# Kernel optimization log

Hardware: AMD Instinct MI355X
Metric: run time of the kernel (lower is better)

The kernel has to match this reference:

```python
import jax, jax.numpy as jnp
import numpy as np

B, T, C = 2, 2048, 1024
N_HEAD, D_HEAD = 16, 64


def setup_inputs() -> dict:
    key = jax.random.key(0)
    k1, k2, k3 = jax.random.split(key, 3)
    scale_in = 1.0 / np.sqrt(C)
    return {
        "x": jax.random.normal(k1, (B, T, C), dtype=jnp.float32),
        "W_attn": jax.random.normal(k2, (C, 3 * C), dtype=jnp.float32) * scale_in,
        "b_attn": jnp.zeros((3 * C,), dtype=jnp.float32),
        "W_proj": jax.random.normal(k3, (C, C), dtype=jnp.float32) * scale_in,
        "b_proj": jnp.zeros((C,), dtype=jnp.float32),
    }


def reference(x, W_attn, b_attn, W_proj, b_proj):
    Bx, Tx, Cx = x.shape
    qkv = x @ W_attn + b_attn                       # [B,T,3C]
    q, k, v = jnp.split(qkv, 3, axis=-1)
    # [B,T,C] -> [B,H,T,Dh]
    q = q.reshape(Bx, Tx, N_HEAD, D_HEAD).transpose(0, 2, 1, 3)
    k = k.reshape(Bx, Tx, N_HEAD, D_HEAD).transpose(0, 2, 1, 3)
    v = v.reshape(Bx, Tx, N_HEAD, D_HEAD).transpose(0, 2, 1, 3)
    att = jnp.einsum("bhqd,bhkd->bhqk", q, k) * (1.0 / jnp.sqrt(D_HEAD))
    causal_mask = jnp.tril(jnp.ones((Tx, Tx), dtype=jnp.bool_))[None, None]
    att = jnp.where(causal_mask, att, -jnp.inf)
    att = jax.nn.softmax(att, axis=-1)
    y = jnp.einsum("bhqk,bhkd->bhqd", att, v)        # [B,H,T,Dh]
    y = y.transpose(0, 2, 1, 3).reshape(Bx, Tx, Cx)  # [B,T,C]
    return y @ W_proj + b_proj
```

## Files before the change

### kernel.cpp

```cpp
#include <hip/hip_runtime.h>

#define BB 2
#define TT 2048
#define CC 1024
#define NHEAD 16
#define DHEAD 64

typedef __attribute__((ext_vector_type(8))) short short8;
typedef __attribute__((ext_vector_type(8))) unsigned short ushort8;
typedef __attribute__((ext_vector_type(4))) float floatx4;
typedef __attribute__((ext_vector_type(2))) unsigned int uintx2;

__device__ inline unsigned short f32_to_bf16_rne(float f) {
  unsigned u = __builtin_bit_cast(unsigned, f);
  unsigned r = (u + 0x7FFFu + ((u >> 16) & 1u)) >> 16;
  return (unsigned short)r;
}
__device__ inline unsigned cvt_pk_bf16(float lo, float hi) {
  unsigned r;
  asm("v_cvt_pk_bf16_f32 %0, %1, %2" : "=v"(r) : "v"(lo), "v"(hi));
  return r;
}
__device__ inline void gload_lds16(const void* g, void* l) {
  __builtin_amdgcn_global_load_lds(
      (const __attribute__((address_space(1))) void*)g,
      (__attribute__((address_space(3))) void*)l, 16, 0, 0);
}

__device__ inline void transpose_tile(const float* __restrict__ W,
                                      unsigned short* __restrict__ Wt,
                                      int K, int N, int scale_cut, float scl,
                                      int bx, int by, float (*T)[33]) {
  const int tx = threadIdx.x & 31;
  const int ty = threadIdx.x >> 5;
  const int r0 = by * 32, c0 = bx * 32;
#pragma unroll
  for (int i = 0; i < 4; ++i)
    T[ty + i * 8][tx] = W[(size_t)(r0 + ty + i * 8) * N + c0 + tx];
  __syncthreads();
#pragma unroll
  for (int i = 0; i < 4; ++i) {
    const int nrow = c0 + ty + i * 8;
    const float s = (nrow < scale_cut) ? scl : 1.0f;
    Wt[(size_t)nrow * K + r0 + tx] = f32_to_bf16_rne(T[tx][ty + i * 8] * s);
  }
}

__global__ __launch_bounds__(256) void prep_kernel(
    const float* __restrict__ x, const float* __restrict__ W_attn,
    const float* __restrict__ b_attn, const float* __restrict__ W_proj,
    unsigned short* __restrict__ xb, unsigned short* __restrict__ Wat,
    unsigned short* __restrict__ Wpt, float* __restrict__ bscl, float scl) {
  __shared__ float T[32][33];
  const int id = blockIdx.x;
  if (id < 4096) {
    const int i = (id * 256 + threadIdx.x) * 4;
    float4 v = *(const float4*)(x + i);
    ushort4 o;
    o.x = f32_to_bf16_rne(v.x);
    o.y = f32_to_bf16_rne(v.y);
    o.z = f32_to_bf16_rne(v.z);
    o.w = f32_to_bf16_rne(v.w);
    *(ushort4*)(xb + i) = o;
  } else if (id < 4096 + 3072) {
    const int t = id - 4096;
    transpose_tile(W_attn, Wat, CC, 3 * CC, CC, scl, t % 96, t / 96, T);
  } else if (id < 4096 + 3072 + 1024) {
    const int t = id - (4096 + 3072);
    transpose_tile(W_proj, Wpt, CC, CC, 0, 1.0f, t % 32, t / 32, T);
  } else {
    const int i = (id - 8192) * 256 + threadIdx.x;
    if (i < 3 * CC) bscl[i] = b_attn[i] * (i < CC ? scl : 1.0f);
  }
}

__global__ __launch_bounds__(256) void transpose_v_kernel(
    const unsigned short* __restrict__ qkv, unsigned short* __restrict__ vT) {
  __shared__ unsigned short Ts[64][72];
  const int tt0 = blockIdx.x * 64;
  const int bh = blockIdx.y;
  const int h = bh & (NHEAD - 1);
  const int b = bh >> 4;
  const int tid = threadIdx.x;
  const unsigned short* src = qkv + (size_t)(b * TT) * (3 * CC) + 2 * CC + h * DHEAD;
#pragma unroll
  for (int it = 0; it < 2; ++it) {
    const int t = it * 32 + (tid >> 3);
    const int d8 = (tid & 7) * 8;
    ushort8 v = *(const ushort8*)(src + (size_t)(tt0 + t) * (3 * CC) + d8);
#pragma unroll
    for (int j = 0; j < 8; ++j) Ts[t][d8 + j] = v[j];
  }
  __syncthreads();
  unsigned short* dst = vT + ((size_t)((b * NHEAD + h) * DHEAD)) * TT;
#pragma unroll
  for (int it = 0; it < 2; ++it) {
    const int d = it * 32 + (tid >> 3);
    const int t8 = (tid & 7) * 8;
    ushort8 o;
#pragma unroll
    for (int j = 0; j < 8; ++j) o[j] = Ts[t8 + j][d];
    *(ushort8*)(dst + (size_t)d * TT + tt0 + t8) = o;
  }
}

__global__ __launch_bounds__(512, 2) void gemm256_kernel(
    const unsigned short* __restrict__ A,
    const unsigned short* __restrict__ Bt,
    const float* __restrict__ bias,
    unsigned short* __restrict__ C,
    int M, int N, int K) {
  __shared__ unsigned short SA[3][256 * 32];
  __shared__ unsigned short SB[3][256 * 32];

  const int id = blockIdx.x;
  const int xcd = id & 7;
  const int j = id >> 3;
  const int row0 = (xcd * 2 + (j >= 12 ? 1 : 0)) * 256;
  const int col0 = (j % 12) * 256;

  const int tid = threadIdx.x;
  const int w = tid >> 6;
  const int lane = tid & 63;
  const int l15 = lane & 15;
  const int l4 = lane >> 4;
  const int wr = (w >> 2) * 128;
  const int wc = (w & 3) * 64;
  const int sr = lane >> 2;
  const int sc = lane & 3;

  floatx4 acc[8][4];
#pragma unroll
  for (int m = 0; m < 8; ++m)
#pragma unroll
    for (int n = 0; n < 4; ++n) acc[m][n] = (floatx4){0.f, 0.f, 0.f, 0.f};

  auto stageA = [&](int t) {
    const int buf = t % 3;
    const int k0 = t * 32;
#pragma unroll
    for (int l = 0; l < 2; ++l) {
      const int r = w * 16 + sr + l * 128;
      gload_lds16(A + (size_t)(row0 + r) * K + k0 + ((sc ^ ((r >> 1) & 3)) * 8),
                  (char*)SA[buf] + (w * 16 + l * 128) * 64);
    }
  };
  auto stageB = [&](int t) {
    const int buf = t % 3;
    const int k0 = t * 32;
#pragma unroll
    for (int l = 0; l < 2; ++l) {
      const int r = w * 16 + sr + l * 128;
      gload_lds16(Bt + (size_t)(col0 + r) * K + k0 + ((sc ^ ((r >> 1) & 3)) * 8),
                  (char*)SB[buf] + (w * 16 + l * 128) * 64);
    }
  };

  stageA(0); stageB(0);
  stageA(1); stageB(1);
  asm volatile("s_waitcnt vmcnt(4)" ::: "memory");
  __builtin_amdgcn_s_barrier();

  const int NT = K / 32;
  for (int t = 0; t < NT; ++t) {
    const unsigned short* sa = SA[t % 3];
    const unsigned short* sb = SB[t % 3];

    short8 af[4], bf[4];
#pragma unroll
    for (int n = 0; n < 4; ++n) {
      const int rb = wc + n * 16 + l15;
      bf[n] = *(const short8*)(sb + rb * 32 + ((l4 ^ ((rb >> 1) & 3)) * 8));
    }
#pragma unroll
    for (int m = 0; m < 4; ++m) {
      const int ra = wr + m * 16 + l15;
      af[m] = *(const short8*)(sa + ra * 32 + ((l4 ^ ((ra >> 1) & 3)) * 8));
    }
    if (t + 2 < NT) stageA(t + 2);
    __builtin_amdgcn_s_barrier();
    __builtin_amdgcn_s_setprio(1);
#pragma unroll
    for (int m = 0; m < 4; ++m)
#pragma unroll
      for (int n = 0; n < 4; ++n)
        acc[m][n] = __builtin_amdgcn_mfma_f32_16x16x32_bf16(af[m], bf[n], acc[m][n], 0, 0, 0);
    __builtin_amdgcn_s_setprio(0);
    __builtin_amdgcn_s_barrier();

#pragma unroll
    for (int m = 0; m < 4; ++m) {
      const int ra = wr + 64 + m * 16 + l15;
      af[m] = *(const short8*)(sa + ra * 32 + ((l4 ^ ((ra >> 1) & 3)) * 8));
    }
    if (t + 2 < NT) stageB(t + 2);
    __builtin_amdgcn_s_barrier();
    __builtin_amdgcn_s_setprio(1);
#pragma unroll
    for (int m = 0; m < 4; ++m)
#pragma unroll
      for (int n = 0; n < 4; ++n)
        acc[4 + m][n] = __builtin_amdgcn_mfma_f32_16x16x32_bf16(af[m], bf[n], acc[4 + m][n], 0, 0, 0);
    __builtin_amdgcn_s_setprio(0);
    __builtin_amdgcn_s_barrier();

    if (t + 1 < NT) {
      if (t + 2 < NT)
        asm volatile("s_waitcnt vmcnt(4)" ::: "memory");
      else
        asm volatile("s_waitcnt vmcnt(0)" ::: "memory");
      __builtin_amdgcn_s_barrier();
    }
  }

  const int rg = l4 * 4;
#pragma unroll
  for (int m = 0; m < 8; ++m) {
#pragma unroll
    for (int n = 0; n < 4; ++n) {
      const int col = col0 + wc + n * 16 + l15;
      const float bv = bias[col];
#pragma unroll
      for (int r = 0; r < 4; ++r) {
        const int row = row0 + wr + m * 16 + rg + r;
        C[(size_t)row * N + col] = f32_to_bf16_rne(acc[m][n][r] + bv);
      }
    }
  }
}

__global__ __launch_bounds__(256) void gemm2_kernel(
    const unsigned short* __restrict__ A,
    const unsigned short* __restrict__ Bt,
    const float* __restrict__ bias,
    float* __restrict__ C,
    int M, int N, int K) {
  __shared__ unsigned short SA[3][128 * 32];
  __shared__ unsigned short SB[3][64 * 32];

  const int id = blockIdx.x;
  const int xcd = id & 7;
  const int j = id >> 3;
  const int col0 = (xcd * 2 + (j >= 32 ? 1 : 0)) * 64;
  const int row0 = (j & 31) * 128;

  const int tid = threadIdx.x;
  const int w = tid >> 6;
  const int lane = tid & 63;
  const int l15 = lane & 15;
  const int l4 = lane >> 4;
  const int wr = (w >> 1) * 64;
  const int wc = (w & 1) * 32;
  const int sr = lane >> 2;
  const int sc = lane & 3;

  floatx4 acc[4][2];
#pragma unroll
  for (int m = 0; m < 4; ++m)
#pragma unroll
    for (int n = 0; n < 2; ++n) acc[m][n] = (floatx4){0.f, 0.f, 0.f, 0.f};

  auto stage = [&](int t) {
    const int buf = t % 3;
    const int k0 = t * 32;
#pragma unroll
    for (int l = 0; l < 2; ++l) {
      const int r = w * 16 + sr + l * 64;
      gload_lds16(A + (size_t)(row0 + r) * K + k0 + ((sc ^ ((r >> 1) & 3)) * 8),
                  (char*)SA[buf] + (w * 16 + l * 64) * 64);
    }
    {
      const int r = w * 16 + sr;
      gload_lds16(Bt + (size_t)(col0 + r) * K + k0 + ((sc ^ ((r >> 1) & 3)) * 8),
                  (char*)SB[buf] + (w * 16) * 64);
    }
  };

  stage(0);
  stage(1);
  asm volatile("s_waitcnt vmcnt(3)" ::: "memory");
  __builtin_amdgcn_s_barrier();

  const int NT = K / 32;
  for (int t = 0; t < NT; ++t) {
    const unsigned short* sa = SA[t % 3];
    const unsigned short* sb = SB[t % 3];

    short8 af[4], bf[2];
#pragma unroll
    for (int n = 0; n < 2; ++n) {
      const int rb = wc + n * 16 + l15;
      bf[n] = *(const short8*)(sb + rb * 32 + ((l4 ^ ((rb >> 1) & 3)) * 8));
    }
#pragma unroll
    for (int m = 0; m < 4; ++m) {
      const int ra = wr + m * 16 + l15;
      af[m] = *(const short8*)(sa + ra * 32 + ((l4 ^ ((ra >> 1) & 3)) * 8));
    }
    if (t + 2 < NT) stage(t + 2);

    __builtin_amdgcn_s_setprio(1);
#pragma unroll
    for (int m = 0; m < 4; ++m)
#pragma unroll
      for (int n = 0; n < 2; ++n)
        acc[m][n] = __builtin_amdgcn_mfma_f32_16x16x32_bf16(af[m], bf[n], acc[m][n], 0, 0, 0);
    __builtin_amdgcn_s_setprio(0);

    if (t + 1 < NT) {
      if (t + 2 < NT)
        asm volatile("s_waitcnt vmcnt(3)" ::: "memory");
      else
        asm volatile("s_waitcnt vmcnt(0)" ::: "memory");
      __builtin_amdgcn_s_barrier();
    }
  }

  const int rg = l4 * 4;
#pragma unroll
  for (int m = 0; m < 4; ++m) {
#pragma unroll
    for (int n = 0; n < 2; ++n) {
      const int col = col0 + wc + n * 16 + l15;
      const float bv = bias[col];
#pragma unroll
      for (int r = 0; r < 4; ++r) {
        const int row = row0 + wr + m * 16 + rg + r;
        C[(size_t)row * N + col] = acc[m][n][r] + bv;
      }
    }
  }
}

__global__ __launch_bounds__(256) void flash_mfma_kernel(
    const unsigned short* __restrict__ qkv,
    const unsigned short* __restrict__ vT,
    unsigned short* __restrict__ y) {
  __shared__ unsigned short Ks[2][64 * 64];
  __shared__ unsigned short Vs[2][64 * 64];
  __shared__ unsigned short Ps[4][16 * 64];

  const int id = blockIdx.x;
  const int xcd = id & 7;
  const int grp = (id >> 3) & 3;
  const int p = id >> 5;
  const int bh = xcd * 4 + grp;
  const int qtA = 31 - p, qtB = p;
  const int ntA = qtA + 1, ntB = qtB + 1;

  const int h = bh & (NHEAD - 1);
  const int b = bh >> 4;
  const int tid = threadIdx.x;
  const int wq = tid >> 6;
  const int lane = tid & 63;
  const int l15 = lane & 15;
  const int l4 = lane >> 4;
  const int srow = lane >> 3;
  const int schunk = lane & 7;

  const size_t baseQ = (size_t)(b * TT) * (3 * CC) + h * DHEAD;
  const size_t baseK = baseQ + CC;
  const size_t vbase = (size_t)((b * NHEAD + h) * DHEAD) * TT;

  short8 aqA[2], aqB[2];
  {
    const unsigned short* qp =
        qkv + baseQ + (size_t)(qtA * 64 + wq * 16 + l15) * (3 * CC) + l4 * 8;
    aqA[0] = *(const short8*)(qp);
    aqA[1] = *(const short8*)(qp + 32);
    const unsigned short* qp2 =
        qkv + baseQ + (size_t)(qtB * 64 + wq * 16 + l15) * (3 * CC) + l4 * 8;
    aqB[0] = *(const short8*)(qp2);
    aqB[1] = *(const short8*)(qp2 + 32);
  }

  floatx4 accT[4];
  float m_i = -1e30f, l_i = 0.f;
#pragma unroll
  for (int n = 0; n < 4; ++n) accT[n] = (floatx4){0.f, 0.f, 0.f, 0.f};

  auto stage = [&](int KT, int BUF) {
#pragma unroll
    for (int it = 0; it < 2; ++it) {
      const int blk = it * 4 + wq;
      const int grow = blk * 8 + srow;
      gload_lds16(qkv + baseK + (size_t)(KT * 64 + grow) * (3 * CC) +
                      (schunk ^ srow) * 8,
                  (char*)Ks[BUF] + blk * 1024);
      gload_lds16(vT + vbase + (size_t)grow * TT + KT * 64 + (schunk ^ srow) * 8,
                  (char*)Vs[BUF] + blk * 1024);
    }
  };

  auto epilogue = [&](int qt) {
    char* Pw = (char*)Ps[wq];
    float lsum = l_i;
    lsum += __shfl_xor(lsum, 16, 64);
    lsum += __shfl_xor(lsum, 32, 64);
    const float inv = 1.0f / lsum;
#pragma unroll
    for (int nd = 0; nd < 4; ++nd) {
      uintx2 dw;
      dw[0] = cvt_pk_bf16(accT[nd][0] * inv, accT[nd][1] * inv);
      dw[1] = cvt_pk_bf16(accT[nd][2] * inv, accT[nd][3] * inv);
      const int c = nd * 2 + (l4 >> 1);
      *(uintx2*)(Pw + l15 * 128 + ((c ^ (l15 & 7)) * 16) + (l4 & 1) * 8) = dw;
    }
    asm volatile("s_waitcnt lgkmcnt(0)" ::: "memory");
#pragma unroll
    for (int ch = 0; ch < 2; ++ch) {
      const int q16 = lane >> 2;
      const int c = ch * 4 + (lane & 3);
      ushort8 o = *(const ushort8*)(Pw + q16 * 128 + ((c ^ (q16 & 7)) * 16));
      const int qg = qt * 64 + wq * 16 + q16;
      *(ushort8*)(y + (size_t)(b * TT + qg) * CC + h * DHEAD + c * 8) = o;
    }
  };

  const int nt_total = ntA + ntB;

  stage(0, 0);
  asm volatile("s_waitcnt vmcnt(0)" ::: "memory");
  __builtin_amdgcn_s_barrier();

  for (int t = 0; t < nt_total; ++t) {
    const bool phB = (t >= ntA);
    const int kt = phB ? t - ntA : t;
    const int qminw = (phB ? qtB : qtA) * 64 + wq * 16;
    const int cur = t & 1;
    if (t + 1 < nt_total)
      stage((t + 1 >= ntA) ? t + 1 - ntA : t + 1, cur ^ 1);

    floatx4 sa[4];
#pragma unroll
    for (int f = 0; f < 4; ++f) sa[f] = (floatx4){0.f, 0.f, 0.f, 0.f};

    __builtin_amdgcn_s_setprio(1);
#pragma unroll
    for (int kc = 0; kc < 2; ++kc) {
      const short8 aq = phB ? aqB[kc] : aqA[kc];
#pragma unroll
      for (int f = 0; f < 4; ++f) {
        const int row = 16 * f + l15;
        short8 bk = *(const short8*)(Ks[cur] + row * 64 +
                                     ((kc * 4 + l4) ^ (row & 7)) * 8);
        sa[f] = __builtin_amdgcn_mfma_f32_16x16x32_bf16(bk, aq, sa[f], 0, 0, 0);
      }
    }
    __builtin_amdgcn_s_setprio(0);

    const int qg = qminw + l15;
    if (kt * 64 + 63 > qminw) {
#pragma unroll
      for (int f = 0; f < 4; ++f)
#pragma unroll
        for (int r = 0; r < 4; ++r) {
          const int kg = kt * 64 + f * 16 + l4 * 4 + r;
          if (kg > qg) sa[f][r] = -1e30f;
        }
    }
    float rm = -1e30f;
#pragma unroll
    for (int f = 0; f < 4; ++f)
      rm = fmaxf(rm, fmaxf(fmaxf(sa[f][0], sa[f][1]), fmaxf(sa[f][2], sa[f][3])));

    float rs = 0.f;
    if (__all(rm <= m_i + 8.0f)) {
#pragma unroll
      for (int f = 0; f < 4; ++f)
#pragma unroll
        for (int r = 0; r < 4; ++r) {
          const float pv = __builtin_amdgcn_exp2f(sa[f][r] - m_i);
          sa[f][r] = pv;
          rs += pv;
        }
      l_i += rs;
    } else {
      rm = fmaxf(rm, __shfl_xor(rm, 16, 64));
      rm = fmaxf(rm, __shfl_xor(rm, 32, 64));
      const float mn = fmaxf(m_i, rm);
      const float scale = __builtin_amdgcn_exp2f(m_i - mn);
#pragma unroll
      for (int f = 0; f < 4; ++f)
#pragma unroll
        for (int r = 0; r < 4; ++r) {
          const float pv = __builtin_amdgcn_exp2f(sa[f][r] - mn);
          sa[f][r] = pv;
          rs += pv;
        }
      l_i = l_i * scale + rs;
      m_i = mn;
#pragma unroll
      for (int nd = 0; nd < 4; ++nd) accT[nd] *= scale;
    }

    char* Pg = (char*)Ps[wq];
#pragma unroll
    for (int f = 0; f < 4; ++f) {
      uintx2 dw;
      dw[0] = cvt_pk_bf16(sa[f][0], sa[f][1]);
      dw[1] = cvt_pk_bf16(sa[f][2], sa[f][3]);
      const int c = f * 2 + (l4 >> 1);
      *(uintx2*)(Pg + l15 * 128 + ((c ^ (l15 & 7)) * 16) + (l4 & 1) * 8) = dw;
    }
    asm volatile("s_waitcnt lgkmcnt(0)" ::: "memory");

    short8 pb[2];
#pragma unroll
    for (int kc = 0; kc < 2; ++kc) {
      const int c = kc * 4 + l4;
      pb[kc] = *(const short8*)(Pg + l15 * 128 + ((c ^ (l15 & 7)) * 16));
    }

    __builtin_amdgcn_s_setprio(1);
#pragma unroll
    for (int kc = 0; kc < 2; ++kc) {
#pragma unroll
      for (int nd = 0; nd < 4; ++nd) {
        const int row = 16 * nd + l15;
        short8 vb = *(const short8*)(Vs[cur] + row * 64 +
                                     ((kc * 4 + l4) ^ (row & 7)) * 8);
        accT[nd] = __builtin_amdgcn_mfma_f32_16x16x32_bf16(vb, pb[kc], accT[nd], 0, 0, 0);
      }
    }
    __builtin_amdgcn_s_setprio(0);

    asm volatile("s_waitcnt vmcnt(0)" ::: "memory");
    __builtin_amdgcn_s_barrier();

    if (t == ntA - 1) {
      epilogue(qtA);
      m_i = -1e30f;
      l_i = 0.f;
#pragma unroll
      for (int n = 0; n < 4; ++n) accT[n] = (floatx4){0.f, 0.f, 0.f, 0.f};
    }
  }

  epilogue(qtB);
}

extern "C" void kernel_launch(void* const* d_in, const int* in_sizes, int n_in,
                              void* d_out, int out_size, void* d_ws, size_t ws_size,
                              hipStream_t stream) {
  const float* x      = (const float*)d_in[0];
  const float* W_attn = (const float*)d_in[1];
  const float* b_attn = (const float*)d_in[2];
  const float* W_proj = (const float*)d_in[3];
  const float* b_proj = (const float*)d_in[4];
  float* out = (float*)d_out;

  const int M = BB * TT;
  const float SCL = 0.125f * 1.44269504089f;

  unsigned short* qkvb = (unsigned short*)d_ws;
  unsigned short* xb   = qkvb + (size_t)M * 3 * CC;
  unsigned short* Wat  = xb + (size_t)M * CC;
  unsigned short* Wpt  = Wat + (size_t)3 * CC * CC;
  unsigned short* yb   = Wpt + (size_t)CC * CC;
  unsigned short* vTb  = yb + (size_t)M * CC;
  float* bscl = (float*)(vTb + (size_t)BB * NHEAD * DHEAD * TT);

  prep_kernel<<<8204, 256, 0, stream>>>(x, W_attn, b_attn, W_proj,
                                        xb, Wat, Wpt, bscl, SCL);

  gemm256_kernel<<<192, 512, 0, stream>>>(xb, Wat, bscl, qkvb, M, 3 * CC, CC);

  {
    dim3 grid(TT / 64, BB * NHEAD);
    transpose_v_kernel<<<grid, 256, 0, stream>>>(qkvb, vTb);
  }

  flash_mfma_kernel<<<512, 256, 0, stream>>>(qkvb, vTb, yb);

  gemm2_kernel<<<512, 256, 0, stream>>>(yb, Wpt, b_proj, out, M, CC, CC);
}
```

Baseline: 116.3 us.

## Retile QKV GEMM to 128x192 blocks with 256 threads and more CTAs

```diff
diff --git a/kernel.cpp b/kernel.cpp
--- a/kernel.cpp
+++ b/kernel.cpp
@@ -104,61 +104,58 @@
   }
 }
 
-__global__ __launch_bounds__(512, 2) void gemm256_kernel(
+__global__ __launch_bounds__(256) void gemm1_kernel(
     const unsigned short* __restrict__ A,
     const unsigned short* __restrict__ Bt,
     const float* __restrict__ bias,
     unsigned short* __restrict__ C,
     int M, int N, int K) {
-  __shared__ unsigned short SA[3][256 * 32];
-  __shared__ unsigned short SB[3][256 * 32];
+  __shared__ unsigned short SA[3][128 * 32];
+  __shared__ unsigned short SB[3][192 * 32];
 
   const int id = blockIdx.x;
   const int xcd = id & 7;
   const int j = id >> 3;
-  const int row0 = (xcd * 2 + (j >= 12 ? 1 : 0)) * 256;
-  const int col0 = (j % 12) * 256;
+  const int row0 = (xcd * 4 + (j >> 4)) * 128;
+  const int col0 = (j & 15) * 192;
 
   const int tid = threadIdx.x;
   const int w = tid >> 6;
   const int lane = tid & 63;
   const int l15 = lane & 15;
   const int l4 = lane >> 4;
-  const int wr = (w >> 2) * 128;
-  const int wc = (w & 3) * 64;
+  const int wr = (w >> 1) * 64;
+  const int wc = (w & 1) * 96;
   const int sr = lane >> 2;
   const int sc = lane & 3;
 
-  floatx4 acc[8][4];
-#pragma unroll
-  for (int m = 0; m < 8; ++m)
-#pragma unroll
-    for (int n = 0; n < 4; ++n) acc[m][n] = (floatx4){0.f, 0.f, 0.f, 0.f};
-
-  auto stageA = [&](int t) {
+  floatx4 acc[4][6];
+#pragma unroll
+  for (int m = 0; m < 4; ++m)
+#pragma unroll
+    for (int n = 0; n < 6; ++n) acc[m][n] = (floatx4){0.f, 0.f, 0.f, 0.f};
+
+  auto stage = [&](int t) {
     const int buf = t % 3;
     const int k0 = t * 32;
 #pragma unroll
-    for (int l = 0; l < 2; ++l) {
-      const int r = w * 16 + sr + l * 128;
-      gload_lds16(A + (size_t)(row0 + r) * K + k0 + ((sc ^ ((r >> 1) & 3)) * 8),
-                  (char*)SA[buf] + (w * 16 + l * 128) * 64);
+    for (int u5 = 0; u5 < 5; ++u5) {
+      const int u = u5 * 4 + w;
+      if (u < 8) {
+        const int r = u * 16 + sr;
+        gload_lds16(A + (size_t)(row0 + r) * K + k0 + ((sc ^ ((r >> 1) & 3)) * 8),
+                    (char*)SA[buf] + u * 1024);
+      } else {
+        const int r = (u - 8) * 16 + sr;
+        gload_lds16(Bt + (size_t)(col0 + r) * K + k0 + ((sc ^ ((r >> 1) & 3)) * 8),
+                    (char*)SB[buf] + (u - 8) * 1024);
+      }
     }
   };
-  auto stageB = [&](int t) {
-    const int buf = t % 3;
-    const int k0 = t * 32;
-#pragma unroll
-    for (int l = 0; l < 2; ++l) {
-      const int r = w * 16 + sr + l * 128;
-      gload_lds16(Bt + (size_t)(col0 + r) * K + k0 + ((sc ^ ((r >> 1) & 3)) * 8),
-                  (char*)SB[buf] + (w * 16 + l * 128) * 64);
-    }
-  };
-
-  stageA(0); stageB(0);
-  stageA(1); stageB(1);
-  asm volatile("s_waitcnt vmcnt(4)" ::: "memory");
+
+  stage(0);
+  stage(1);
+  asm volatile("s_waitcnt vmcnt(5)" ::: "memory");
   __builtin_amdgcn_s_barrier();
 
   const int NT = K / 32;
@@ -166,9 +163,9 @@
     const unsigned short* sa = SA[t % 3];
     const unsigned short* sb = SB[t % 3];
 
-    short8 af[4], bf[4];
-#pragma unroll
-    for (int n = 0; n < 4; ++n) {
+    short8 af[4], bf[6];
+#pragma unroll
+    for (int n = 0; n < 6; ++n) {
       const int rb = wc + n * 16 + l15;
       bf[n] = *(const short8*)(sb + rb * 32 + ((l4 ^ ((rb >> 1) & 3)) * 8));
     }
@@ -177,36 +174,19 @@
       const int ra = wr + m * 16 + l15;
       af[m] = *(const short8*)(sa + ra * 32 + ((l4 ^ ((ra >> 1) & 3)) * 8));
     }
-    if (t + 2 < NT) stageA(t + 2);
-    __builtin_amdgcn_s_barrier();
+    if (t + 2 < NT) stage(t + 2);
+
     __builtin_amdgcn_s_setprio(1);
 #pragma unroll
     for (int m = 0; m < 4; ++m)
 #pragma unroll
-      for (int n = 0; n < 4; ++n)
+      for (int n = 0; n < 6; ++n)
         acc[m][n] = __builtin_amdgcn_mfma_f32_16x16x32_bf16(af[m], bf[n], acc[m][n], 0, 0, 0);
     __builtin_amdgcn_s_setprio(0);
-    __builtin_amdgcn_s_barrier();
-
-#pragma unroll
-    for (int m = 0; m < 4; ++m) {
-      const int ra = wr + 64 + m * 16 + l15;
-      af[m] = *(const short8*)(sa + ra * 32 + ((l4 ^ ((ra >> 1) & 3)) * 8));
-    }
-    if (t + 2 < NT) stageB(t + 2);
-    __builtin_amdgcn_s_barrier();
-    __builtin_amdgcn_s_setprio(1);
-#pragma unroll
-    for (int m = 0; m < 4; ++m)
-#pragma unroll
-      for (int n = 0; n < 4; ++n)
-        acc[4 + m][n] = __builtin_amdgcn_mfma_f32_16x16x32_bf16(af[m], bf[n], acc[4 + m][n], 0, 0, 0);
-    __builtin_amdgcn_s_setprio(0);
-    __builtin_amdgcn_s_barrier();
 
     if (t + 1 < NT) {
       if (t + 2 < NT)
-        asm volatile("s_waitcnt vmcnt(4)" ::: "memory");
+        asm volatile("s_waitcnt vmcnt(5)" ::: "memory");
       else
         asm volatile("s_waitcnt vmcnt(0)" ::: "memory");
       __builtin_amdgcn_s_barrier();
@@ -215,9 +195,9 @@
 
   const int rg = l4 * 4;
 #pragma unroll
-  for (int m = 0; m < 8; ++m) {
-#pragma unroll
-    for (int n = 0; n < 4; ++n) {
+  for (int m = 0; m < 4; ++m) {
+#pragma unroll
+    for (int n = 0; n < 6; ++n) {
       const int col = col0 + wc + n * 16 + l15;
       const float bv = bias[col];
 #pragma unroll
@@ -564,7 +544,7 @@
   prep_kernel<<<8204, 256, 0, stream>>>(x, W_attn, b_attn, W_proj,
                                         xb, Wat, Wpt, bscl, SCL);
 
-  gemm256_kernel<<<192, 512, 0, stream>>>(xb, Wat, bscl, qkvb, M, 3 * CC, CC);
+  gemm1_kernel<<<512, 256, 0, stream>>>(xb, Wat, bscl, qkvb, M, 3 * CC, CC);
 
   {
     dim3 grid(TT / 64, BB * NHEAD);
```

Measured after the change: 108.1 us. 1.08x faster.
